# Kernel optimization log

Measured on AMD Instinct MI355X. Metric: run time of the kernel, lower is better.

## Reference

```python
import jax, jax.numpy as jnp
import numpy as np

ATT_H = 256
DEC_H = 512
CTX = 1024  # 2 * encoder_hidden_size


def setup_inputs() -> dict:
    key = jax.random.key(0)
    ks = jax.random.split(key, 8)
    B, T = 32, 4096
    prev = jax.random.normal(ks[0], (B, 1, DEC_H), dtype=jnp.float32)
    enc = jax.random.normal(ks[1], (B, T, CTX), dtype=jnp.float32)
    # nn.Linear params: weight [out,in], bias [out]
    W_w = jax.random.normal(ks[2], (ATT_H, DEC_H), dtype=jnp.float32) / np.sqrt(DEC_H)
    W_b = jax.random.normal(ks[3], (ATT_H,), dtype=jnp.float32) * 0.01
    U_w = jax.random.normal(ks[4], (ATT_H, CTX), dtype=jnp.float32) / np.sqrt(CTX)
    U_b = jax.random.normal(ks[5], (ATT_H,), dtype=jnp.float32) * 0.01
    v = jax.random.uniform(ks[6], (ATT_H,), dtype=jnp.float32)
    return {
        "batch_size": B,
        "max_seq_len": T,
        "previous_decoder_hidden_state": prev,
        "encoder_final_hidden_layers": enc,
        "W_w": W_w, "W_b": W_b, "U_w": U_w, "U_b": U_b, "v": v,
    }


def reference(batch_size, max_seq_len, previous_decoder_hidden_state,
              encoder_final_hidden_layers, W_w, W_b, U_w, U_b, v):
    # tmp_1: [B,1,H] = W(prev); tmp_3: [B,T,H] = U(enc)
    tmp1 = jnp.einsum('bod,hd->boh', previous_decoder_hidden_state, W_w) + W_b
    tmp3 = jnp.einsum('btc,hc->bth', encoder_final_hidden_layers, U_w) + U_b
    # energy: [B,T] = relu(tmp1 + tmp3) . v
    energy = jnp.einsum('bth,h->bt', jax.nn.relu(tmp1 + tmp3), v)
    alpha = jax.nn.softmax(energy, axis=1)  # [B,T]
    # weighted sum over time -> context [B, 2E]
    c = jnp.einsum('bt,btc->bc', alpha, encoder_final_hidden_layers)
    return c
```

## Files before the change

kernel.cpp:

```cpp
#include <hip/hip_runtime.h>
#include <hip/hip_bf16.h>

#define BB   32
#define TT   4096
#define CTXD 1024
#define HH   256
#define DH   512
#define BT   64
#define NTILES (TT/BT)
#define BK   64
#define LDA  72

typedef __attribute__((ext_vector_type(8))) short bf16x8;
typedef __attribute__((ext_vector_type(4))) float f32x4;

static __device__ __forceinline__ unsigned short f2bf(float f) {
    unsigned int u = __float_as_uint(f);
    u += 0x7FFF + ((u >> 16) & 1);
    return (unsigned short)(u >> 16);
}

__global__ void uconv_kernel(const float* __restrict__ Uw, unsigned short* __restrict__ Ub) {
    int idx = blockIdx.x * blockDim.x + threadIdx.x;
    float4 u4 = ((const float4*)Uw)[idx];
    ushort4 o;
    o.x = f2bf(u4.x); o.y = f2bf(u4.y); o.z = f2bf(u4.z); o.w = f2bf(u4.w);
    ((ushort4*)Ub)[idx] = o;
}

__global__ void bias_kernel(const float* __restrict__ prev, const float* __restrict__ Ww,
                            const float* __restrict__ Wb, const float* __restrict__ Ubias,
                            float* __restrict__ bias) {
    __shared__ float ps[DH];
    int b = blockIdx.x, h = threadIdx.x;
    if (h < DH / 4) ((float4*)ps)[h] = ((const float4*)(prev + (size_t)b * DH))[h];
    __syncthreads();
    float acc = Wb[h] + Ubias[h];
    const float4* wr = (const float4*)(Ww + (size_t)h * DH);
    #pragma unroll 4
    for (int d = 0; d < DH / 4; ++d) {
        float4 w4 = wr[d];
        float4 p4 = ((const float4*)ps)[d];
        acc += w4.x * p4.x + w4.y * p4.y + w4.z * p4.z + w4.w * p4.w;
    }
    bias[b * HH + h] = acc;
}

__global__ void attn_main(const float* __restrict__ enc, const unsigned short* __restrict__ Ub,
                          const float* __restrict__ bias, const float* __restrict__ v,
                          float* __restrict__ partO, float* __restrict__ partM,
                          float* __restrict__ partL) {
    __shared__ __align__(16) unsigned short As[BT * LDA];
    __shared__ __align__(16) unsigned short Us[HH * LDA];
    __shared__ float epart[4][BT];
    __shared__ float pbuf[BT];

    const int tid  = threadIdx.x;
    const int lane = tid & 63;
    const int w    = tid >> 6;
    const int quad = lane >> 4;
    const int l15  = lane & 15;
    const int b    = blockIdx.x & 31;
    const int tile = blockIdx.x >> 5;
    const int t0   = tile * BT;
    const int pi   = b * NTILES + tile;

    const float* encBase = enc + ((size_t)b * TT + t0) * CTXD;

    f32x4 acc[4][4];
    #pragma unroll
    for (int mi = 0; mi < 4; ++mi)
        #pragma unroll
        for (int ni = 0; ni < 4; ++ni) acc[mi][ni] = (f32x4){0.f, 0.f, 0.f, 0.f};

    const int arow = tid >> 4;
    const int acg  = tid & 15;

    for (int kt = 0; kt < CTXD / BK; ++kt) {
        const float* ga = encBase + kt * BK;
        #pragma unroll
        for (int rr = 0; rr < 4; ++rr) {
            int row = arow + rr * 16;
            float4 a4 = *(const float4*)(ga + (size_t)row * CTXD + acg * 4);
            ushort4 o;
            o.x = f2bf(a4.x); o.y = f2bf(a4.y); o.z = f2bf(a4.z); o.w = f2bf(a4.w);
            *(ushort4*)&As[row * LDA + acg * 4] = o;
        }
        #pragma unroll
        for (int ii = 0; ii < 8; ++ii) {
            int idx = ii * 256 + tid;
            int row = idx >> 3;
            int g   = idx & 7;
            uint4 u = *(const uint4*)(Ub + (size_t)row * CTXD + kt * BK + g * 8);
            *(uint4*)&Us[row * LDA + g * 8] = u;
        }
        __syncthreads();
        #pragma unroll
        for (int ks = 0; ks < BK / 32; ++ks) {
            bf16x8 af[4], bfr[4];
            #pragma unroll
            for (int mi = 0; mi < 4; ++mi)
                af[mi] = *(const bf16x8*)&As[(mi * 16 + l15) * LDA + ks * 32 + quad * 8];
            #pragma unroll
            for (int ni = 0; ni < 4; ++ni)
                bfr[ni] = *(const bf16x8*)&Us[(w * 64 + ni * 16 + l15) * LDA + ks * 32 + quad * 8];
            #pragma unroll
            for (int mi = 0; mi < 4; ++mi)
                #pragma unroll
                for (int ni = 0; ni < 4; ++ni)
                    acc[mi][ni] = __builtin_amdgcn_mfma_f32_16x16x32_bf16(af[mi], bfr[ni], acc[mi][ni], 0, 0, 0);
        }
        __syncthreads();
    }

    float vv[4], bb[4];
    #pragma unroll
    for (int ni = 0; ni < 4; ++ni) {
        int h = w * 64 + ni * 16 + l15;
        vv[ni] = v[h];
        bb[ni] = bias[b * HH + h];
    }
    #pragma unroll
    for (int mi = 0; mi < 4; ++mi) {
        #pragma unroll
        for (int r = 0; r < 4; ++r) {
            float e = 0.f;
            #pragma unroll
            for (int ni = 0; ni < 4; ++ni) {
                float x = acc[mi][ni][r] + bb[ni];
                e += fmaxf(x, 0.f) * vv[ni];
            }
            e += __shfl_xor(e, 1);
            e += __shfl_xor(e, 2);
            e += __shfl_xor(e, 4);
            e += __shfl_xor(e, 8);
            if (l15 == 0) epart[w][mi * 16 + quad * 4 + r] = e;
        }
    }
    __syncthreads();

    if (tid < 64) {
        float e = epart[0][tid] + epart[1][tid] + epart[2][tid] + epart[3][tid];
        float m = e;
        #pragma unroll
        for (int off = 32; off; off >>= 1) m = fmaxf(m, __shfl_xor(m, off));
        float p = __expf(e - m);
        float l = p;
        #pragma unroll
        for (int off = 32; off; off >>= 1) l += __shfl_xor(l, off);
        pbuf[tid] = p;
        if (tid == 0) { partM[pi] = m; partL[pi] = l; }
    }
    __syncthreads();

    float4 o4 = {0.f, 0.f, 0.f, 0.f};
    #pragma unroll 4
    for (int t = 0; t < BT; ++t) {
        float p = pbuf[t];
        float4 ev = *(const float4*)(encBase + (size_t)t * CTXD + tid * 4);
        o4.x += p * ev.x; o4.y += p * ev.y; o4.z += p * ev.z; o4.w += p * ev.w;
    }
    *(float4*)(partO + (size_t)pi * CTXD + tid * 4) = o4;
}

__global__ void combine_kernel(const float* __restrict__ partO, const float* __restrict__ partM,
                               const float* __restrict__ partL, float* __restrict__ out) {
    __shared__ float sc[NTILES];
    __shared__ float sL;
    int b = blockIdx.x, tid = threadIdx.x;
    if (tid < 64) {
        float m = partM[b * NTILES + tid];
        float l = partL[b * NTILES + tid];
        float M = m;
        #pragma unroll
        for (int off = 32; off; off >>= 1) M = fmaxf(M, __shfl_xor(M, off));
        float s = __expf(m - M);
        sc[tid] = s;
        float Lp = l * s;
        #pragma unroll
        for (int off = 32; off; off >>= 1) Lp += __shfl_xor(Lp, off);
        if (tid == 0) sL = Lp;
    }
    __syncthreads();
    float4 o = {0.f, 0.f, 0.f, 0.f};
    const float* base = partO + (size_t)b * NTILES * CTXD;
    #pragma unroll 4
    for (int i = 0; i < NTILES; ++i) {
        float s = sc[i];
        float4 p4 = *(const float4*)(base + (size_t)i * CTXD + tid * 4);
        o.x += s * p4.x; o.y += s * p4.y; o.z += s * p4.z; o.w += s * p4.w;
    }
    float inv = 1.0f / sL;
    float4 r; r.x = o.x * inv; r.y = o.y * inv; r.z = o.z * inv; r.w = o.w * inv;
    ((float4*)out)[b * (CTXD / 4) + tid] = r;
}

extern "C" void kernel_launch(void* const* d_in, const int* in_sizes, int n_in,
                              void* d_out, int out_size, void* d_ws, size_t ws_size,
                              hipStream_t stream) {
    const float* prev  = (const float*)d_in[2];
    const float* enc   = (const float*)d_in[3];
    const float* Ww    = (const float*)d_in[4];
    const float* Wb    = (const float*)d_in[5];
    const float* Uw    = (const float*)d_in[6];
    const float* Ubias = (const float*)d_in[7];
    const float* v     = (const float*)d_in[8];
    float* out = (float*)d_out;

    char* ws = (char*)d_ws;
    float* bias          = (float*)ws;
    unsigned short* Ub   = (unsigned short*)(ws + 32768);
    float* partO         = (float*)(ws + 32768 + 524288);
    float* partM         = partO + (size_t)BB * NTILES * CTXD;
    float* partL         = partM + BB * NTILES;

    uconv_kernel<<<dim3(256), dim3(256), 0, stream>>>(Uw, Ub);
    bias_kernel<<<dim3(BB), dim3(HH), 0, stream>>>(prev, Ww, Wb, Ubias, bias);
    attn_main<<<dim3(BB * NTILES), dim3(256), 0, stream>>>(enc, Ub, bias, v, partO, partM, partL);
    combine_kernel<<<dim3(BB), dim3(256), 0, stream>>>(partO, partM, partL, out);
}
```

Baseline: 864.2 us.

## Keep bf16 encoder tile resident in LDS and prefetch next K-slice in registers

The attention kernel now stores the whole 64x1024 bf16 encoder tile in dynamic LDS. It reuses that tile for the softmax-weighted context sum instead of re-reading fp32 encoder rows from global memory. The K loop uses BK=32 with a register double-buffer: the next slice's global loads are issued before the current slice is stored to LDS and fed to the MFMAs. The cost is a large LDS footprint (about 150 KB), which limits the kernel to one block and four waves per CU. The context sum also now uses bf16-rounded encoder values, which may reduce accuracy.

```diff
diff --git a/kernel.cpp b/kernel.cpp
--- a/kernel.cpp
+++ b/kernel.cpp
@@ -8,8 +8,11 @@
 #define DH   512
 #define BT   64
 #define NTILES (TT/BT)
-#define BK   64
-#define LDA  72
+#define BK   32
+#define NKT  (CTXD/BK)
+#define LDA  1032
+#define LDU  40
+#define SMEM_BYTES (BT*LDA*2 + HH*LDU*2 + 4*BT*4 + BT*4)
 
 typedef __attribute__((ext_vector_type(8))) short bf16x8;
 typedef __attribute__((ext_vector_type(4))) float f32x4;
@@ -18,6 +21,12 @@
     unsigned int u = __float_as_uint(f);
     u += 0x7FFF + ((u >> 16) & 1);
     return (unsigned short)(u >> 16);
+}
+static __device__ __forceinline__ unsigned pack2(float x, float y) {
+    return (unsigned)f2bf(x) | ((unsigned)f2bf(y) << 16);
+}
+static __device__ __forceinline__ float bf2f(unsigned short u) {
+    return __uint_as_float((unsigned)u << 16);
 }
 
 __global__ void uconv_kernel(const float* __restrict__ Uw, unsigned short* __restrict__ Ub) {
@@ -46,14 +55,16 @@
     bias[b * HH + h] = acc;
 }
 
-__global__ void attn_main(const float* __restrict__ enc, const unsigned short* __restrict__ Ub,
-                          const float* __restrict__ bias, const float* __restrict__ v,
-                          float* __restrict__ partO, float* __restrict__ partM,
-                          float* __restrict__ partL) {
-    __shared__ __align__(16) unsigned short As[BT * LDA];
-    __shared__ __align__(16) unsigned short Us[HH * LDA];
-    __shared__ float epart[4][BT];
-    __shared__ float pbuf[BT];
+__global__ __launch_bounds__(256, 1)
+void attn_main(const float* __restrict__ enc, const unsigned short* __restrict__ Ub,
+               const float* __restrict__ bias, const float* __restrict__ v,
+               float* __restrict__ partO, float* __restrict__ partM,
+               float* __restrict__ partL) {
+    extern __shared__ __align__(16) char smem[];
+    unsigned short* As = (unsigned short*)smem;
+    unsigned short* Us = (unsigned short*)(smem + BT * LDA * 2);
+    float* epart = (float*)(smem + BT * LDA * 2 + HH * LDU * 2);
+    float* pbuf  = epart + 4 * BT;
 
     const int tid  = threadIdx.x;
     const int lane = tid & 63;
@@ -65,7 +76,10 @@
     const int t0   = tile * BT;
     const int pi   = b * NTILES + tile;
 
-    const float* encBase = enc + ((size_t)b * TT + t0) * CTXD;
+    const int srow = tid >> 2;
+    const int sg   = tid & 3;
+    const float*          gA = enc + ((size_t)b * TT + t0 + srow) * CTXD + sg * 8;
+    const unsigned short* gU = Ub + (size_t)srow * CTXD + sg * 8;
 
     f32x4 acc[4][4];
     #pragma unroll
@@ -73,44 +87,47 @@
         #pragma unroll
         for (int ni = 0; ni < 4; ++ni) acc[mi][ni] = (f32x4){0.f, 0.f, 0.f, 0.f};
 
-    const int arow = tid >> 4;
-    const int acg  = tid & 15;
-
-    for (int kt = 0; kt < CTXD / BK; ++kt) {
-        const float* ga = encBase + kt * BK;
-        #pragma unroll
-        for (int rr = 0; rr < 4; ++rr) {
-            int row = arow + rr * 16;
-            float4 a4 = *(const float4*)(ga + (size_t)row * CTXD + acg * 4);
-            ushort4 o;
-            o.x = f2bf(a4.x); o.y = f2bf(a4.y); o.z = f2bf(a4.z); o.w = f2bf(a4.w);
-            *(ushort4*)&As[row * LDA + acg * 4] = o;
-        }
-        #pragma unroll
-        for (int ii = 0; ii < 8; ++ii) {
-            int idx = ii * 256 + tid;
-            int row = idx >> 3;
-            int g   = idx & 7;
-            uint4 u = *(const uint4*)(Ub + (size_t)row * CTXD + kt * BK + g * 8);
-            *(uint4*)&Us[row * LDA + g * 8] = u;
-        }
+    float4 ca0 = *(const float4*)(gA);
+    float4 ca1 = *(const float4*)(gA + 4);
+    uint4  cu0 = *(const uint4*)(gU);
+    uint4  cu1 = *(const uint4*)(gU + (size_t)64 * CTXD);
+    uint4  cu2 = *(const uint4*)(gU + (size_t)128 * CTXD);
+    uint4  cu3 = *(const uint4*)(gU + (size_t)192 * CTXD);
+
+    for (int kt = 0; kt < NKT; ++kt) {
+        int ktn = (kt + 1 < NKT) ? kt + 1 : kt;
+        float4 na0 = *(const float4*)(gA + ktn * BK);
+        float4 na1 = *(const float4*)(gA + ktn * BK + 4);
+        uint4  nu0 = *(const uint4*)(gU + ktn * BK);
+        uint4  nu1 = *(const uint4*)(gU + (size_t)64 * CTXD + ktn * BK);
+        uint4  nu2 = *(const uint4*)(gU + (size_t)128 * CTXD + ktn * BK);
+        uint4  nu3 = *(const uint4*)(gU + (size_t)192 * CTXD + ktn * BK);
+
         __syncthreads();
-        #pragma unroll
-        for (int ks = 0; ks < BK / 32; ++ks) {
-            bf16x8 af[4], bfr[4];
-            #pragma unroll
-            for (int mi = 0; mi < 4; ++mi)
-                af[mi] = *(const bf16x8*)&As[(mi * 16 + l15) * LDA + ks * 32 + quad * 8];
+        uint4 pa;
+        pa.x = pack2(ca0.x, ca0.y); pa.y = pack2(ca0.z, ca0.w);
+        pa.z = pack2(ca1.x, ca1.y); pa.w = pack2(ca1.z, ca1.w);
+        *(uint4*)&As[srow * LDA + kt * BK + sg * 8] = pa;
+        *(uint4*)&Us[(srow      ) * LDU + sg * 8] = cu0;
+        *(uint4*)&Us[(srow +  64) * LDU + sg * 8] = cu1;
+        *(uint4*)&Us[(srow + 128) * LDU + sg * 8] = cu2;
+        *(uint4*)&Us[(srow + 192) * LDU + sg * 8] = cu3;
+        __syncthreads();
+
+        bf16x8 af[4], bfr[4];
+        #pragma unroll
+        for (int mi = 0; mi < 4; ++mi)
+            af[mi] = *(const bf16x8*)&As[(mi * 16 + l15) * LDA + kt * BK + quad * 8];
+        #pragma unroll
+        for (int ni = 0; ni < 4; ++ni)
+            bfr[ni] = *(const bf16x8*)&Us[(w * 64 + ni * 16 + l15) * LDU + quad * 8];
+        #pragma unroll
+        for (int mi = 0; mi < 4; ++mi)
             #pragma unroll
             for (int ni = 0; ni < 4; ++ni)
-                bfr[ni] = *(const bf16x8*)&Us[(w * 64 + ni * 16 + l15) * LDA + ks * 32 + quad * 8];
-            #pragma unroll
-            for (int mi = 0; mi < 4; ++mi)
-                #pragma unroll
-                for (int ni = 0; ni < 4; ++ni)
-                    acc[mi][ni] = __builtin_amdgcn_mfma_f32_16x16x32_bf16(af[mi], bfr[ni], acc[mi][ni], 0, 0, 0);
-        }
-        __syncthreads();
+                acc[mi][ni] = __builtin_amdgcn_mfma_f32_16x16x32_bf16(af[mi], bfr[ni], acc[mi][ni], 0, 0, 0);
+
+        ca0 = na0; ca1 = na1; cu0 = nu0; cu1 = nu1; cu2 = nu2; cu3 = nu3;
     }
 
     float vv[4], bb[4];
@@ -134,13 +151,13 @@
             e += __shfl_xor(e, 2);
             e += __shfl_xor(e, 4);
             e += __shfl_xor(e, 8);
-            if (l15 == 0) epart[w][mi * 16 + quad * 4 + r] = e;
+            if (l15 == 0) epart[w * BT + mi * 16 + quad * 4 + r] = e;
         }
     }
     __syncthreads();
 
     if (tid < 64) {
-        float e = epart[0][tid] + epart[1][tid] + epart[2][tid] + epart[3][tid];
+        float e = epart[0 * BT + tid] + epart[1 * BT + tid] + epart[2 * BT + tid] + epart[3 * BT + tid];
         float m = e;
         #pragma unroll
         for (int off = 32; off; off >>= 1) m = fmaxf(m, __shfl_xor(m, off));
@@ -153,14 +170,19 @@
     }
     __syncthreads();
 
-    float4 o4 = {0.f, 0.f, 0.f, 0.f};
-    #pragma unroll 4
+    const int c4 = tid * 4;
+    float o0 = 0.f, o1 = 0.f, o2 = 0.f, o3 = 0.f;
+    #pragma unroll 8
     for (int t = 0; t < BT; ++t) {
         float p = pbuf[t];
-        float4 ev = *(const float4*)(encBase + (size_t)t * CTXD + tid * 4);
-        o4.x += p * ev.x; o4.y += p * ev.y; o4.z += p * ev.z; o4.w += p * ev.w;
-    }
-    *(float4*)(partO + (size_t)pi * CTXD + tid * 4) = o4;
+        ushort4 e4 = *(const ushort4*)&As[t * LDA + c4];
+        o0 += p * bf2f(e4.x);
+        o1 += p * bf2f(e4.y);
+        o2 += p * bf2f(e4.z);
+        o3 += p * bf2f(e4.w);
+    }
+    float4 r4; r4.x = o0; r4.y = o1; r4.z = o2; r4.w = o3;
+    *(float4*)(partO + (size_t)pi * CTXD + c4) = r4;
 }
 
 __global__ void combine_kernel(const float* __restrict__ partO, const float* __restrict__ partM,
@@ -214,8 +236,13 @@
     float* partM         = partO + (size_t)BB * NTILES * CTXD;
     float* partL         = partM + BB * NTILES;
 
+    static int lds_set = 0;
+    hipFuncSetAttribute((const void*)attn_main,
+                        hipFuncAttributeMaxDynamicSharedMemorySize, SMEM_BYTES);
+    (void)lds_set;
+
     uconv_kernel<<<dim3(256), dim3(256), 0, stream>>>(Uw, Ub);
     bias_kernel<<<dim3(BB), dim3(HH), 0, stream>>>(prev, Ww, Wb, Ubias, bias);
-    attn_main<<<dim3(BB * NTILES), dim3(256), 0, stream>>>(enc, Ub, bias, v, partO, partM, partL);
+    attn_main<<<dim3(BB * NTILES), dim3(256), SMEM_BYTES, stream>>>(enc, Ub, bias, v, partO, partM, partL);
     combine_kernel<<<dim3(BB), dim3(256), 0, stream>>>(partO, partM, partL, out);
 }
```

Measured after the change: 864.9 us. About the same (+0.1%).
